# Optimization experiments

Measured on AMD Instinct MI355X. Metric: run time of the kernel, lower is better.

## Reference

```python
import jax, jax.numpy as jnp
import numpy as np

D_IN, D, N_HEADS, K, VOCAB = 768, 512, 8, 6, 1000
HEAD_DIM = D // N_HEADS


def setup_inputs() -> dict:
    key = jax.random.key(0)
    ks = jax.random.split(key, 16)
    B, T, L = 32, 4096, 512
    s = 0.02
    return {
        "video_features": jax.random.normal(ks[0], (B, T, D_IN), jnp.float32),
        "input_ids": jax.random.randint(ks[1], (B, L), 0, VOCAB),
        "attention_mask": jnp.ones((B, L), jnp.float32),
        # video_encoder (Linear 768->512), stored [in, out]
        "W_enc": jax.random.normal(ks[2], (D_IN, D), jnp.float32) * s,
        "b_enc": jnp.zeros((D,), jnp.float32),
        # frame_selector (Linear 512->1)
        "W_sel": jax.random.normal(ks[3], (D, 1), jnp.float32) * s,
        "b_sel": jnp.zeros((1,), jnp.float32),
        # text_encoder embedding
        "emb": jax.random.normal(ks[4], (VOCAB, D), jnp.float32) * s,
        # MultiheadAttention in/out projections
        "W_q": jax.random.normal(ks[5], (D, D), jnp.float32) * s,
        "W_k": jax.random.normal(ks[6], (D, D), jnp.float32) * s,
        "W_v": jax.random.normal(ks[7], (D, D), jnp.float32) * s,
        "b_q": jnp.zeros((D,), jnp.float32),
        "b_k": jnp.zeros((D,), jnp.float32),
        "b_v": jnp.zeros((D,), jnp.float32),
        "W_o": jax.random.normal(ks[8], (D, D), jnp.float32) * s,
        "b_o": jnp.zeros((D,), jnp.float32),
        # classifier (Linear 512->1000)
        "W_cls": jax.random.normal(ks[9], (D, VOCAB), jnp.float32) * s,
        "b_cls": jnp.zeros((VOCAB,), jnp.float32),
    }


def reference(video_features, input_ids, attention_mask, W_enc, b_enc, W_sel,
              b_sel, emb, W_q, W_k, W_v, b_q, b_k, b_v, W_o, b_o, W_cls, b_cls):
    # encode frames: [B, T, 512]
    ve = jax.nn.relu(jnp.einsum('bti,io->bto', video_features, W_enc) + b_enc)
    # frame scores [B, T] -> top-6 gather
    scores = jnp.einsum('btd,do->bto', ve, W_sel)[..., 0] + b_sel[0]
    _, top_idx = jax.lax.top_k(scores, K)                      # [B, K]
    reps = jnp.take_along_axis(ve, top_idx[:, :, None], axis=1)  # [B, K, 512]
    # text embedding (query), reps as key/value
    txt = emb[input_ids]                                       # [B, L, 512]
    B, L, _ = txt.shape
    q = (txt @ W_q + b_q).reshape(B, L, N_HEADS, HEAD_DIM)
    k = (reps @ W_k + b_k).reshape(B, K, N_HEADS, HEAD_DIM)
    v = (reps @ W_v + b_v).reshape(B, K, N_HEADS, HEAD_DIM)
    scale = 1.0 / np.sqrt(HEAD_DIM).astype(np.float32)
    attn = jax.nn.softmax(jnp.einsum('blhd,bkhd->bhlk', q, k) * scale, axis=-1)
    ctx = jnp.einsum('bhlk,bkhd->blhd', attn, v).reshape(B, L, D)
    fused = ctx @ W_o + b_o
    logits = fused @ W_cls + b_cls                             # [B, L, 1000]
    return logits, reps
```

## Files before the change

### kernel.cpp

```cpp
#include <hip/hip_runtime.h>
#include <math.h>


#define DEV __device__ __forceinline__

typedef _Float16 half8 __attribute__((ext_vector_type(8)));
typedef float f32x4v __attribute__((ext_vector_type(4)));

DEV unsigned short f2h_bits(float f) {
  union { _Float16 h; unsigned short u; } cv;
  cv.h = (_Float16)f;
  return cv.u;
}

DEV void gload16(const void* g, void* lds) {
  auto* gp = reinterpret_cast<const __attribute__((address_space(1))) unsigned int*>(
      reinterpret_cast<unsigned long long>(g));
  auto* lp = reinterpret_cast<__attribute__((address_space(3))) unsigned int*>(
      reinterpret_cast<unsigned long long>(lds));
  __builtin_amdgcn_global_load_lds(gp, lp, 16, 0, 0);
}

__global__ __launch_bounds__(256) void wenct_k(const float* __restrict__ W_enc,
                                               unsigned short* __restrict__ WencT) {
  __shared__ unsigned short t[64][65];
  const int k0 = blockIdx.x * 64, n0 = blockIdx.y * 64, tid = threadIdx.x;
  for (int e = tid; e < 4096; e += 256) {
    int kk = e >> 6, nn = e & 63;
    t[kk][nn] = f2h_bits(W_enc[(size_t)(k0 + kk) * 512 + n0 + nn]);
  }
  __syncthreads();
  for (int e = tid; e < 4096; e += 256) {
    int nn = e >> 6, kk = e & 63;
    WencT[(size_t)(n0 + nn) * 768 + k0 + kk] = t[kk][nn];
  }
}

__global__ __launch_bounds__(512, 2) void score_gemm(
    const float* __restrict__ vf, const unsigned short* __restrict__ WencT,
    const float* __restrict__ b_enc, const float* __restrict__ W_sel,
    const float* __restrict__ b_sel, float* __restrict__ scores) {
  __shared__ unsigned short As[128 * 64];
  __shared__ unsigned short Bs[512 * 64];
  __shared__ float red[8 * 128];

  const int tid = threadIdx.x;
  const int w = tid >> 6, lane = tid & 63;
  const int quad = lane >> 4, l15 = lane & 15;
  const int rowBase = blockIdx.x * 128;
  const int swz = l15 & 7;
  char* const AsB = (char*)As;
  char* const BsB = (char*)Bs;

  f32x4v acc[8][4];
#pragma unroll
  for (int i = 0; i < 8; ++i)
#pragma unroll
    for (int j = 0; j < 4; ++j) acc[i][j] = (f32x4v){0.f, 0.f, 0.f, 0.f};

  const int ar0 = tid >> 3, as0 = tid & 7;

  for (int kk = 0; kk < 12; ++kk) {
    const int k0 = kk * 64;
    __syncthreads();
#pragma unroll
    for (int it = 0; it < 8; ++it) {
      int q = tid + it * 512;
      int n = q >> 3, seg = q & 7;
      gload16(WencT + (size_t)n * 768 + k0 + ((seg ^ (n & 7)) << 3),
              BsB + (it * 512 + w * 64) * 16);
    }
#pragma unroll
    for (int h = 0; h < 2; ++h) {
      int row = ar0 + h * 64;
      const float* src = vf + (size_t)(rowBase + row) * 768 + k0 + as0 * 8;
      float4 fa = *(const float4*)src;
      float4 fb = *(const float4*)(src + 4);
      uint4 pk;
      pk.x = f2h_bits(fa.x) | ((unsigned int)f2h_bits(fa.y) << 16);
      pk.y = f2h_bits(fa.z) | ((unsigned int)f2h_bits(fa.w) << 16);
      pk.z = f2h_bits(fb.x) | ((unsigned int)f2h_bits(fb.y) << 16);
      pk.w = f2h_bits(fb.z) | ((unsigned int)f2h_bits(fb.w) << 16);
      *(uint4*)(AsB + row * 128 + ((as0 ^ (row & 7)) << 4)) = pk;
    }
    __syncthreads();
#pragma unroll
    for (int c = 0; c < 2; ++c) {
      half8 af[8], bfr[4];
      const int so = (((c << 2) | quad) ^ swz) << 4;
#pragma unroll
      for (int i = 0; i < 8; ++i)
        af[i] = *(const half8*)(AsB + (16 * i + l15) * 128 + so);
#pragma unroll
      for (int j = 0; j < 4; ++j)
        bfr[j] = *(const half8*)(BsB + (w * 64 + 16 * j + l15) * 128 + so);
#pragma unroll
      for (int i = 0; i < 8; ++i)
#pragma unroll
        for (int j = 0; j < 4; ++j)
          acc[i][j] = __builtin_amdgcn_mfma_f32_16x16x32_f16(af[i], bfr[j], acc[i][j], 0, 0, 0);
    }
  }

  float be[4], wsv[4];
#pragma unroll
  for (int j = 0; j < 4; ++j) {
    int col = w * 64 + 16 * j + l15;
    be[j] = b_enc[col];
    wsv[j] = W_sel[col];
  }
  float part[32];
#pragma unroll
  for (int x = 0; x < 32; ++x) part[x] = 0.f;
#pragma unroll
  for (int i = 0; i < 8; ++i)
#pragma unroll
    for (int j = 0; j < 4; ++j)
#pragma unroll
      for (int r = 0; r < 4; ++r) {
        float v = acc[i][j][r] + be[j];
        v = fmaxf(v, 0.f);
        part[i * 4 + r] += v * wsv[j];
      }
#pragma unroll
  for (int m = 1; m < 16; m <<= 1)
#pragma unroll
    for (int x = 0; x < 32; ++x) part[x] += __shfl_xor(part[x], m);
  if (l15 == 0) {
#pragma unroll
    for (int i = 0; i < 8; ++i)
#pragma unroll
      for (int r = 0; r < 4; ++r)
        red[w * 128 + 16 * i + quad * 4 + r] = part[i * 4 + r];
  }
  __syncthreads();
  if (tid < 128) {
    float s = 0.f;
#pragma unroll
    for (int ww = 0; ww < 8; ++ww) s += red[ww * 128 + tid];
    scores[rowBase + tid] = s + b_sel[0];
  }
}

__global__ __launch_bounds__(256) void topk16(const float* __restrict__ scores,
                                              int* __restrict__ cand) {
  __shared__ float swv[4];
  __shared__ int swi[4];
  __shared__ int winner;
  const int b = blockIdx.x, tid = threadIdx.x;
  const int lane = tid & 63, w = tid >> 6;
  float v[16];
#pragma unroll
  for (int p = 0; p < 16; ++p) v[p] = scores[b * 4096 + p * 256 + tid];
  for (int r = 0; r < 16; ++r) {
    float bv = v[0];
    int bp = 0;
#pragma unroll
    for (int p = 1; p < 16; ++p)
      if (v[p] > bv) { bv = v[p]; bp = p; }
    int bi = bp * 256 + tid;
#pragma unroll
    for (int m = 1; m < 64; m <<= 1) {
      float ov = __shfl_xor(bv, m);
      int oi = __shfl_xor(bi, m);
      if (ov > bv || (ov == bv && oi < bi)) { bv = ov; bi = oi; }
    }
    if (lane == 0) { swv[w] = bv; swi[w] = bi; }
    __syncthreads();
    if (tid == 0) {
      float fv = swv[0];
      int fi = swi[0];
#pragma unroll
      for (int x = 1; x < 4; ++x)
        if (swv[x] > fv || (swv[x] == fv && swi[x] < fi)) { fv = swv[x]; fi = swi[x]; }
      cand[b * 16 + r] = fi;
      winner = fi;
    }
    __syncthreads();
    const int wi = winner;
    const int wp = wi >> 8, wt = wi & 255;
#pragma unroll
    for (int p = 0; p < 16; ++p)
      if (p == wp && tid == wt) v[p] = -3.0e38f;
    __syncthreads();
  }
}

__global__ __launch_bounds__(256) void rescore(
    const float* __restrict__ vf, const int* __restrict__ cand,
    const float* __restrict__ W_enc, const float* __restrict__ b_enc,
    const float* __restrict__ W_sel, const float* __restrict__ b_sel,
    float* __restrict__ veC, float* __restrict__ exsc) {
  __shared__ float vfs[4][768];
  __shared__ float redl[16];
  const int b = blockIdx.x, cb = blockIdx.y * 4, tid = threadIdx.x;
  for (int c = 0; c < 4; ++c) {
    int t = cand[b * 16 + cb + c];
    const float* src = vf + ((size_t)b * 4096 + t) * 768;
    for (int i = tid; i < 768; i += 256) vfs[c][i] = src[i];
  }
  __syncthreads();
  const int j0 = tid, j1 = tid + 256;
  float a0[4] = {0.f, 0.f, 0.f, 0.f}, a1[4] = {0.f, 0.f, 0.f, 0.f};
  for (int i = 0; i < 768; ++i) {
    float w0 = W_enc[(size_t)i * 512 + j0], w1 = W_enc[(size_t)i * 512 + j1];
#pragma unroll
    for (int c = 0; c < 4; ++c) {
      float x = vfs[c][i];
      a0[c] += x * w0;
      a1[c] += x * w1;
    }
  }
  float ws0 = W_sel[j0], ws1 = W_sel[j1];
  float be0 = b_enc[j0], be1 = b_enc[j1];
  float s[4];
#pragma unroll
  for (int c = 0; c < 4; ++c) {
    float v0 = fmaxf(a0[c] + be0, 0.f);
    float v1 = fmaxf(a1[c] + be1, 0.f);
    veC[((size_t)b * 16 + cb + c) * 512 + j0] = v0;
    veC[((size_t)b * 16 + cb + c) * 512 + j1] = v1;
    s[c] = v0 * ws0 + v1 * ws1;
  }
#pragma unroll
  for (int m = 1; m < 64; m <<= 1)
#pragma unroll
    for (int c = 0; c < 4; ++c) s[c] += __shfl_xor(s[c], m);
  int w = tid >> 6;
  if ((tid & 63) == 0) {
#pragma unroll
    for (int c = 0; c < 4; ++c) redl[c * 4 + w] = s[c];
  }
  __syncthreads();
  if (tid < 4)
    exsc[b * 16 + cb + tid] = redl[tid * 4 + 0] + redl[tid * 4 + 1] +
                              redl[tid * 4 + 2] + redl[tid * 4 + 3] + b_sel[0];
}

__global__ __launch_bounds__(256) void select6(
    const float* __restrict__ exsc, const int* __restrict__ cand,
    const float* __restrict__ veC, int* __restrict__ sel,
    float* __restrict__ repsOut) {
  __shared__ int selL[6];
  const int b = blockIdx.x, tid = threadIdx.x;
  if (tid == 0) {
    float v[16]; int idx[16]; bool used[16];
    for (int c = 0; c < 16; ++c) {
      v[c] = exsc[b * 16 + c];
      idx[c] = cand[b * 16 + c];
      used[c] = false;
    }
    for (int r = 0; r < 6; ++r) {
      int bi = -1;
      for (int c = 0; c < 16; ++c) {
        if (used[c]) continue;
        if (bi < 0 || v[c] > v[bi] || (v[c] == v[bi] && idx[c] < idx[bi])) bi = c;
      }
      used[bi] = true;
      selL[r] = bi;
      sel[b * 6 + r] = bi;
    }
  }
  __syncthreads();
  for (int r = 0; r < 6; ++r) {
    int c = selL[r];
    for (int i = tid; i < 512; i += 256)
      repsOut[((size_t)b * 6 + r) * 512 + i] = veC[((size_t)b * 16 + c) * 512 + i];
  }
}

__global__ __launch_bounds__(256) void kv_proj(
    const int* __restrict__ sel, const float* __restrict__ veC,
    const float* __restrict__ W_k, const float* __restrict__ W_v,
    const float* __restrict__ b_k, const float* __restrict__ b_v,
    float* __restrict__ Ks, float* __restrict__ Vs) {
  __shared__ float rep[512];
  const int br = blockIdx.x;
  const int b = br / 6;
  const int tid = threadIdx.x;
  const int c = sel[br];
  for (int i = tid; i < 512; i += 256) rep[i] = veC[((size_t)b * 16 + c) * 512 + i];
  __syncthreads();
  const int j0 = tid, j1 = tid + 256;
  float k0 = 0.f, k1 = 0.f, v0 = 0.f, v1 = 0.f;
  for (int m = 0; m < 512; ++m) {
    float x = rep[m];
    k0 += x * W_k[m * 512 + j0];
    k1 += x * W_k[m * 512 + j1];
    v0 += x * W_v[m * 512 + j0];
    v1 += x * W_v[m * 512 + j1];
  }
  Ks[(size_t)br * 512 + j0] = (k0 + b_k[j0]) * 0.125f;
  Ks[(size_t)br * 512 + j1] = (k1 + b_k[j1]) * 0.125f;
  Vs[(size_t)br * 512 + j0] = v0 + b_v[j0];
  Vs[(size_t)br * 512 + j1] = v1 + b_v[j1];
}

__global__ __launch_bounds__(256) void qemb_k(
    const float* __restrict__ emb, const float* __restrict__ W_q,
    const float* __restrict__ b_q, float* __restrict__ Qe) {
  __shared__ float er[4 * 512];
  const int r0 = blockIdx.x * 4, tid = threadIdx.x;
  for (int i = tid; i < 2048; i += 256) er[i] = emb[(size_t)r0 * 512 + i];
  __syncthreads();
  const int j0 = tid, j1 = tid + 256;
  float a0[4], a1[4];
#pragma unroll
  for (int r = 0; r < 4; ++r) { a0[r] = 0.f; a1[r] = 0.f; }
  for (int i = 0; i < 512; ++i) {
    float w0 = W_q[i * 512 + j0], w1 = W_q[i * 512 + j1];
#pragma unroll
    for (int r = 0; r < 4; ++r) {
      a0[r] += er[r * 512 + i] * w0;
      a1[r] += er[r * 512 + i] * w1;
    }
  }
  float bq0 = b_q[j0], bq1 = b_q[j1];
#pragma unroll
  for (int r = 0; r < 4; ++r) {
    Qe[(size_t)(r0 + r) * 512 + j0] = a0[r] + bq0;
    Qe[(size_t)(r0 + r) * 512 + j1] = a1[r] + bq1;
  }
}

__global__ __launch_bounds__(256) void woc_k(
    const float* __restrict__ W_o, const float* __restrict__ W_cls,
    unsigned short* __restrict__ WocT) {
  __shared__ float wr[4 * 512];
  const int i0 = blockIdx.x * 4, tid = threadIdx.x;
  for (int i = tid; i < 2048; i += 256) wr[i] = W_o[(size_t)i0 * 512 + i];
  __syncthreads();
  float a[4][4];
#pragma unroll
  for (int r = 0; r < 4; ++r)
#pragma unroll
    for (int c = 0; c < 4; ++c) a[r][c] = 0.f;
  for (int m = 0; m < 512; ++m) {
    float wc[4];
#pragma unroll
    for (int c = 0; c < 4; ++c) {
      int j = tid + c * 256;
      wc[c] = (j < 1000) ? W_cls[(size_t)m * 1000 + j] : 0.f;
    }
#pragma unroll
    for (int r = 0; r < 4; ++r) {
      float x = wr[r * 512 + m];
#pragma unroll
      for (int c = 0; c < 4; ++c) a[r][c] += x * wc[c];
    }
  }
#pragma unroll
  for (int r = 0; r < 4; ++r)
#pragma unroll
    for (int c = 0; c < 4; ++c) {
      int j = tid + c * 256;
      if (j < 1000) WocT[(size_t)j * 512 + i0 + r] = f2h_bits(a[r][c]);
    }
  if (blockIdx.x == 0) {
    for (int i = tid; i < 24 * 512; i += 256) WocT[512000 + i] = 0;
  }
}

__global__ void boc_k(const float* __restrict__ b_o, const float* __restrict__ W_cls,
                      const float* __restrict__ b_cls, float* __restrict__ boc) {
  int j = blockIdx.x * 256 + threadIdx.x;
  float s = 0.f;
  if (j < 1000) {
    for (int m = 0; m < 512; ++m) s += b_o[m] * W_cls[(size_t)m * 1000 + j];
    s += b_cls[j];
  }
  boc[j] = s;
}

__global__ __launch_bounds__(256) void ctx_kernel(
    const int* __restrict__ ids, const float* __restrict__ Qe,
    const float* __restrict__ Ks, const float* __restrict__ Vs,
    unsigned short* __restrict__ CTX) {
  const int token = blockIdx.x * 4 + (threadIdx.x >> 6);
  const int lane = threadIdx.x & 63;
  const int b = token >> 9;
  const int id = ids[token];
  float q[8];
#pragma unroll
  for (int h = 0; h < 8; ++h) q[h] = Qe[(size_t)id * 512 + h * 64 + lane];
  float s[8][6];
#pragma unroll
  for (int kk = 0; kk < 6; ++kk) {
    const float* kp = Ks + ((size_t)b * 6 + kk) * 512 + lane;
    float p[8];
#pragma unroll
    for (int h = 0; h < 8; ++h) p[h] = q[h] * kp[h * 64];
#pragma unroll
    for (int m = 1; m < 64; m <<= 1)
#pragma unroll
      for (int h = 0; h < 8; ++h) p[h] += __shfl_xor(p[h], m);
#pragma unroll
    for (int h = 0; h < 8; ++h) s[h][kk] = p[h];
  }
  const float* vbase = Vs + (size_t)b * 6 * 512 + lane;
#pragma unroll
  for (int h = 0; h < 8; ++h) {
    float mx = s[h][0];
#pragma unroll
    for (int kk = 1; kk < 6; ++kk) mx = fmaxf(mx, s[h][kk]);
    float e[6], sum = 0.f;
#pragma unroll
    for (int kk = 0; kk < 6; ++kk) { e[kk] = __expf(s[h][kk] - mx); sum += e[kk]; }
    float c = 0.f;
#pragma unroll
    for (int kk = 0; kk < 6; ++kk) c += e[kk] * vbase[(size_t)kk * 512 + h * 64];
    c *= (1.f / sum);
    CTX[(size_t)token * 512 + h * 64 + lane] = f2h_bits(c);
  }
}

__global__ __launch_bounds__(512, 2) void logits_gemm(
    const unsigned short* __restrict__ CTX, const unsigned short* __restrict__ WocT,
    const float* __restrict__ boc, float* __restrict__ out) {
  __shared__ unsigned short As[128 * 64];
  __shared__ unsigned short Bs[512 * 64];
  const int tid = threadIdx.x;
  const int w = tid >> 6, lane = tid & 63;
  const int quad = lane >> 4, l15 = lane & 15;
  const int rowBase = blockIdx.x * 128;
  const int n0 = blockIdx.y * 512;
  const int swz = l15 & 7;
  char* const AsB = (char*)As;
  char* const BsB = (char*)Bs;

  f32x4v acc[8][4];
#pragma unroll
  for (int i = 0; i < 8; ++i)
#pragma unroll
    for (int j = 0; j < 4; ++j) acc[i][j] = (f32x4v){0.f, 0.f, 0.f, 0.f};

  for (int kk = 0; kk < 8; ++kk) {
    const int k0 = kk * 64;
    __syncthreads();
#pragma unroll
    for (int h = 0; h < 2; ++h) {
      int u = tid + h * 512;
      int row = u >> 3, seg = u & 7;
      gload16(CTX + (size_t)(rowBase + row) * 512 + k0 + ((seg ^ (row & 7)) << 3),
              AsB + (h * 512 + w * 64) * 16);
    }
#pragma unroll
    for (int it = 0; it < 8; ++it) {
      int q = tid + it * 512;
      int n = q >> 3, seg = q & 7;
      gload16(WocT + (size_t)(n0 + n) * 512 + k0 + ((seg ^ (n & 7)) << 3),
              BsB + (it * 512 + w * 64) * 16);
    }
    __syncthreads();
#pragma unroll
    for (int c = 0; c < 2; ++c) {
      half8 af[8], bfr[4];
      const int so = (((c << 2) | quad) ^ swz) << 4;
#pragma unroll
      for (int i = 0; i < 8; ++i)
        af[i] = *(const half8*)(AsB + (16 * i + l15) * 128 + so);
#pragma unroll
      for (int j = 0; j < 4; ++j)
        bfr[j] = *(const half8*)(BsB + (w * 64 + 16 * j + l15) * 128 + so);
#pragma unroll
      for (int i = 0; i < 8; ++i)
#pragma unroll
        for (int j = 0; j < 4; ++j)
          acc[i][j] = __builtin_amdgcn_mfma_f32_16x16x32_f16(af[i], bfr[j], acc[i][j], 0, 0, 0);
    }
  }

  float bo[4];
#pragma unroll
  for (int j = 0; j < 4; ++j) bo[j] = boc[n0 + w * 64 + 16 * j + l15];
#pragma unroll
  for (int i = 0; i < 8; ++i)
#pragma unroll
    for (int j = 0; j < 4; ++j)
#pragma unroll
      for (int r = 0; r < 4; ++r) {
        int token = rowBase + 16 * i + quad * 4 + r;
        int col = n0 + w * 64 + 16 * j + l15;
        if (col < 1000) out[(size_t)token * 1000 + col] = acc[i][j][r] + bo[j];
      }
}

extern "C" void kernel_launch(void* const* d_in, const int* in_sizes, int n_in,
                              void* d_out, int out_size, void* d_ws, size_t ws_size,
                              hipStream_t stream) {
  (void)in_sizes; (void)n_in; (void)out_size; (void)ws_size;
  const float* vf    = (const float*)d_in[0];
  const int*   ids   = (const int*)d_in[1];
  const float* W_enc = (const float*)d_in[3];
  const float* b_enc = (const float*)d_in[4];
  const float* W_sel = (const float*)d_in[5];
  const float* b_sel = (const float*)d_in[6];
  const float* emb   = (const float*)d_in[7];
  const float* W_q   = (const float*)d_in[8];
  const float* W_k   = (const float*)d_in[9];
  const float* W_v   = (const float*)d_in[10];
  const float* b_q   = (const float*)d_in[11];
  const float* b_k   = (const float*)d_in[12];
  const float* b_v   = (const float*)d_in[13];
  const float* W_o   = (const float*)d_in[14];
  const float* b_o   = (const float*)d_in[15];
  const float* W_cls = (const float*)d_in[16];
  const float* b_cls = (const float*)d_in[17];

  float* out = (float*)d_out;
  float* reps_out = out + (size_t)16384000;

  char* p = (char*)d_ws;
  auto nxt = [&](size_t bytes) -> char* {
    char* q = p;
    p += (bytes + 255) & ~(size_t)255;
    return q;
  };
  unsigned short* WencT = (unsigned short*)nxt((size_t)512 * 768 * 2);
  unsigned short* WocT  = (unsigned short*)nxt((size_t)1024 * 512 * 2);
  unsigned short* CTX   = (unsigned short*)nxt((size_t)16384 * 512 * 2);
  float* scores = (float*)nxt((size_t)131072 * 4);
  int*   cand   = (int*)nxt((size_t)512 * 4);
  float* exsc   = (float*)nxt((size_t)512 * 4);
  float* veC    = (float*)nxt((size_t)32 * 16 * 512 * 4);
  int*   sel    = (int*)nxt((size_t)192 * 4);
  float* Ks     = (float*)nxt((size_t)98304 * 4);
  float* Vs     = (float*)nxt((size_t)98304 * 4);
  float* Qe     = (float*)nxt((size_t)512000 * 4);
  float* boc    = (float*)nxt((size_t)1024 * 4);

  hipLaunchKernelGGL(wenct_k,     dim3(12, 8),  dim3(256), 0, stream, W_enc, WencT);
  hipLaunchKernelGGL(score_gemm,  dim3(1024),   dim3(512), 0, stream, vf, WencT, b_enc, W_sel, b_sel, scores);
  hipLaunchKernelGGL(topk16,      dim3(32),     dim3(256), 0, stream, scores, cand);
  hipLaunchKernelGGL(rescore,     dim3(32, 4),  dim3(256), 0, stream, vf, cand, W_enc, b_enc, W_sel, b_sel, veC, exsc);
  hipLaunchKernelGGL(select6,     dim3(32),     dim3(256), 0, stream, exsc, cand, veC, sel, reps_out);
  hipLaunchKernelGGL(kv_proj,     dim3(192),    dim3(256), 0, stream, sel, veC, W_k, W_v, b_k, b_v, Ks, Vs);
  hipLaunchKernelGGL(qemb_k,      dim3(250),    dim3(256), 0, stream, emb, W_q, b_q, Qe);
  hipLaunchKernelGGL(woc_k,       dim3(128),    dim3(256), 0, stream, W_o, W_cls, WocT);
  hipLaunchKernelGGL(boc_k,       dim3(4),      dim3(256), 0, stream, b_o, W_cls, b_cls, boc);
  hipLaunchKernelGGL(ctx_kernel,  dim3(4096),   dim3(256), 0, stream, ids, Qe, Ks, Vs, CTX);
  hipLaunchKernelGGL(logits_gemm, dim3(128, 2), dim3(512), 0, stream, CTX, WocT, boc, out);
}
```

Baseline: 1.092 ms.

## Fuse prep and selection kernels, double-buffer both MFMA GEMMs with K=32 stages

```diff
diff --git a/kernel.cpp b/kernel.cpp
--- a/kernel.cpp
+++ b/kernel.cpp
@@ -11,6 +11,15 @@
   union { _Float16 h; unsigned short u; } cv;
   cv.h = (_Float16)f;
   return cv.u;
+}
+
+DEV uint4 packf16x8(float4 fa, float4 fb) {
+  uint4 pk;
+  pk.x = (unsigned int)f2h_bits(fa.x) | ((unsigned int)f2h_bits(fa.y) << 16);
+  pk.y = (unsigned int)f2h_bits(fa.z) | ((unsigned int)f2h_bits(fa.w) << 16);
+  pk.z = (unsigned int)f2h_bits(fb.x) | ((unsigned int)f2h_bits(fb.y) << 16);
+  pk.w = (unsigned int)f2h_bits(fb.z) | ((unsigned int)f2h_bits(fb.w) << 16);
+  return pk;
 }
 
 DEV void gload16(const void* g, void* lds) {
@@ -21,18 +30,92 @@
   __builtin_amdgcn_global_load_lds(gp, lp, 16, 0, 0);
 }
 
-__global__ __launch_bounds__(256) void wenct_k(const float* __restrict__ W_enc,
-                                               unsigned short* __restrict__ WencT) {
-  __shared__ unsigned short t[64][65];
-  const int k0 = blockIdx.x * 64, n0 = blockIdx.y * 64, tid = threadIdx.x;
-  for (int e = tid; e < 4096; e += 256) {
-    int kk = e >> 6, nn = e & 63;
-    t[kk][nn] = f2h_bits(W_enc[(size_t)(k0 + kk) * 512 + n0 + nn]);
-  }
-  __syncthreads();
-  for (int e = tid; e < 4096; e += 256) {
-    int nn = e >> 6, kk = e & 63;
-    WencT[(size_t)(n0 + nn) * 768 + k0 + kk] = t[kk][nn];
+__global__ __launch_bounds__(256) void prep_k(
+    const float* __restrict__ W_enc, unsigned short* __restrict__ WencT,
+    const float* __restrict__ emb, const float* __restrict__ W_q,
+    const float* __restrict__ b_q, float* __restrict__ Qe,
+    const float* __restrict__ W_o, const float* __restrict__ W_cls,
+    unsigned short* __restrict__ WocT, const float* __restrict__ b_o,
+    const float* __restrict__ b_cls, float* __restrict__ boc) {
+  __shared__ float plds[2080];
+  const int blk = blockIdx.x, tid = threadIdx.x;
+  if (blk < 96) {
+    unsigned short* t = (unsigned short*)plds;
+    const int k0 = (blk % 12) * 64, n0 = (blk / 12) * 64;
+    for (int e = tid; e < 4096; e += 256) {
+      int kk = e >> 6, nn = e & 63;
+      t[kk * 65 + nn] = f2h_bits(W_enc[(size_t)(k0 + kk) * 512 + n0 + nn]);
+    }
+    __syncthreads();
+    for (int e = tid; e < 4096; e += 256) {
+      int nn = e >> 6, kk = e & 63;
+      WencT[(size_t)(n0 + nn) * 768 + k0 + kk] = t[kk * 65 + nn];
+    }
+  } else if (blk < 346) {
+    float* er = plds;
+    const int r0 = (blk - 96) * 4;
+    for (int i = tid; i < 2048; i += 256) er[i] = emb[(size_t)r0 * 512 + i];
+    __syncthreads();
+    const int j0 = tid, j1 = tid + 256;
+    float a0[4], a1[4];
+#pragma unroll
+    for (int r = 0; r < 4; ++r) { a0[r] = 0.f; a1[r] = 0.f; }
+    for (int i = 0; i < 512; ++i) {
+      float w0 = W_q[i * 512 + j0], w1 = W_q[i * 512 + j1];
+#pragma unroll
+      for (int r = 0; r < 4; ++r) {
+        a0[r] += er[r * 512 + i] * w0;
+        a1[r] += er[r * 512 + i] * w1;
+      }
+    }
+    float bq0 = b_q[j0], bq1 = b_q[j1];
+#pragma unroll
+    for (int r = 0; r < 4; ++r) {
+      Qe[(size_t)(r0 + r) * 512 + j0] = a0[r] + bq0;
+      Qe[(size_t)(r0 + r) * 512 + j1] = a1[r] + bq1;
+    }
+  } else if (blk < 474) {
+    float* wr = plds;
+    const int i0 = (blk - 346) * 4;
+    for (int i = tid; i < 2048; i += 256) wr[i] = W_o[(size_t)i0 * 512 + i];
+    __syncthreads();
+    float a[4][4];
+#pragma unroll
+    for (int r = 0; r < 4; ++r)
+#pragma unroll
+      for (int c = 0; c < 4; ++c) a[r][c] = 0.f;
+    for (int m = 0; m < 512; ++m) {
+      float wc[4];
+#pragma unroll
+      for (int c = 0; c < 4; ++c) {
+        int j = tid + c * 256;
+        wc[c] = (j < 1000) ? W_cls[(size_t)m * 1000 + j] : 0.f;
+      }
+#pragma unroll
+      for (int r = 0; r < 4; ++r) {
+        float x = wr[r * 512 + m];
+#pragma unroll
+        for (int c = 0; c < 4; ++c) a[r][c] += x * wc[c];
+      }
+    }
+#pragma unroll
+    for (int r = 0; r < 4; ++r)
+#pragma unroll
+      for (int c = 0; c < 4; ++c) {
+        int j = tid + c * 256;
+        if (j < 1000) WocT[(size_t)j * 512 + i0 + r] = f2h_bits(a[r][c]);
+      }
+    if (blk == 346) {
+      for (int i = tid; i < 24 * 512; i += 256) WocT[512000 + i] = 0;
+    }
+  } else {
+    int j = (blk - 474) * 256 + tid;
+    float s = 0.f;
+    if (j < 1000) {
+      for (int m = 0; m < 512; ++m) s += b_o[m] * W_cls[(size_t)m * 1000 + j];
+      s += b_cls[j];
+    }
+    boc[j] = s;
   }
 }
 
@@ -40,17 +123,19 @@
     const float* __restrict__ vf, const unsigned short* __restrict__ WencT,
     const float* __restrict__ b_enc, const float* __restrict__ W_sel,
     const float* __restrict__ b_sel, float* __restrict__ scores) {
-  __shared__ unsigned short As[128 * 64];
-  __shared__ unsigned short Bs[512 * 64];
+  __shared__ unsigned short As[2][128 * 32];
+  __shared__ unsigned short Bs[2][512 * 32];
   __shared__ float red[8 * 128];
 
   const int tid = threadIdx.x;
-  const int w = tid >> 6, lane = tid & 63;
+  const int wv = tid >> 6, lane = tid & 63;
   const int quad = lane >> 4, l15 = lane & 15;
   const int rowBase = blockIdx.x * 128;
-  const int swz = l15 & 7;
-  char* const AsB = (char*)As;
-  char* const BsB = (char*)Bs;
+  const int rso = ((quad ^ (l15 & 3)) << 4);
+  char* const AsB0 = (char*)As[0];
+  char* const AsB1 = (char*)As[1];
+  char* const BsB0 = (char*)Bs[0];
+  char* const BsB1 = (char*)Bs[1];
 
   f32x4v acc[8][4];
 #pragma unroll
@@ -58,54 +143,60 @@
 #pragma unroll
     for (int j = 0; j < 4; ++j) acc[i][j] = (f32x4v){0.f, 0.f, 0.f, 0.f};
 
-  const int ar0 = tid >> 3, as0 = tid & 7;
-
-  for (int kk = 0; kk < 12; ++kk) {
-    const int k0 = kk * 64;
-    __syncthreads();
-#pragma unroll
-    for (int it = 0; it < 8; ++it) {
+  const int arow = tid >> 2, aseg = tid & 3;
+  const float* aSrc = vf + (size_t)(rowBase + arow) * 768 + aseg * 8;
+  const int adst = arow * 64 + ((aseg ^ (arow & 3)) << 4);
+
+  auto stage_b = [&](int kk, char* dstB) {
+#pragma unroll
+    for (int it = 0; it < 4; ++it) {
       int q = tid + it * 512;
-      int n = q >> 3, seg = q & 7;
-      gload16(WencT + (size_t)n * 768 + k0 + ((seg ^ (n & 7)) << 3),
-              BsB + (it * 512 + w * 64) * 16);
-    }
-#pragma unroll
-    for (int h = 0; h < 2; ++h) {
-      int row = ar0 + h * 64;
-      const float* src = vf + (size_t)(rowBase + row) * 768 + k0 + as0 * 8;
-      float4 fa = *(const float4*)src;
-      float4 fb = *(const float4*)(src + 4);
-      uint4 pk;
-      pk.x = f2h_bits(fa.x) | ((unsigned int)f2h_bits(fa.y) << 16);
-      pk.y = f2h_bits(fa.z) | ((unsigned int)f2h_bits(fa.w) << 16);
-      pk.z = f2h_bits(fb.x) | ((unsigned int)f2h_bits(fb.y) << 16);
-      pk.w = f2h_bits(fb.z) | ((unsigned int)f2h_bits(fb.w) << 16);
-      *(uint4*)(AsB + row * 128 + ((as0 ^ (row & 7)) << 4)) = pk;
-    }
-    __syncthreads();
-#pragma unroll
-    for (int c = 0; c < 2; ++c) {
-      half8 af[8], bfr[4];
-      const int so = (((c << 2) | quad) ^ swz) << 4;
-#pragma unroll
-      for (int i = 0; i < 8; ++i)
-        af[i] = *(const half8*)(AsB + (16 * i + l15) * 128 + so);
+      int n = q >> 2, seg = q & 3;
+      gload16(WencT + (size_t)n * 768 + kk * 32 + ((seg ^ (n & 3)) << 3),
+              dstB + (it * 512 + wv * 64) * 16);
+    }
+  };
+  auto consume = [&](const char* A, const char* B) {
+    half8 af[8], bf[4];
+#pragma unroll
+    for (int i = 0; i < 8; ++i)
+      af[i] = *(const half8*)(A + (16 * i + l15) * 64 + rso);
+#pragma unroll
+    for (int j = 0; j < 4; ++j)
+      bf[j] = *(const half8*)(B + (wv * 64 + 16 * j + l15) * 64 + rso);
+#pragma unroll
+    for (int i = 0; i < 8; ++i)
 #pragma unroll
       for (int j = 0; j < 4; ++j)
-        bfr[j] = *(const half8*)(BsB + (w * 64 + 16 * j + l15) * 128 + so);
-#pragma unroll
-      for (int i = 0; i < 8; ++i)
-#pragma unroll
-        for (int j = 0; j < 4; ++j)
-          acc[i][j] = __builtin_amdgcn_mfma_f32_16x16x32_f16(af[i], bfr[j], acc[i][j], 0, 0, 0);
-    }
-  }
+        acc[i][j] = __builtin_amdgcn_mfma_f32_16x16x32_f16(af[i], bf[j], acc[i][j], 0, 0, 0);
+  };
+
+  stage_b(0, BsB0);
+  {
+    float4 fa = *(const float4*)(aSrc);
+    float4 fb = *(const float4*)(aSrc + 4);
+    *(uint4*)(AsB0 + adst) = packf16x8(fa, fb);
+  }
+  __syncthreads();
+  int cur = 0;
+  for (int kk = 0; kk < 23; ++kk) {
+    const float* s = aSrc + (kk + 1) * 32;
+    float4 fa = *(const float4*)(s);
+    float4 fb = *(const float4*)(s + 4);
+    char* An = cur ? AsB0 : AsB1;
+    char* Bn = cur ? BsB0 : BsB1;
+    stage_b(kk + 1, Bn);
+    consume(cur ? AsB1 : AsB0, cur ? BsB1 : BsB0);
+    *(uint4*)(An + adst) = packf16x8(fa, fb);
+    __syncthreads();
+    cur ^= 1;
+  }
+  consume(cur ? AsB1 : AsB0, cur ? BsB1 : BsB0);
 
   float be[4], wsv[4];
 #pragma unroll
   for (int j = 0; j < 4; ++j) {
-    int col = w * 64 + 16 * j + l15;
+    int col = wv * 64 + 16 * j + l15;
     be[j] = b_enc[col];
     wsv[j] = W_sel[col];
   }
@@ -131,7 +222,7 @@
     for (int i = 0; i < 8; ++i)
 #pragma unroll
       for (int r = 0; r < 4; ++r)
-        red[w * 128 + 16 * i + quad * 4 + r] = part[i * 4 + r];
+        red[wv * 128 + 16 * i + quad * 4 + r] = part[i * 4 + r];
   }
   __syncthreads();
   if (tid < 128) {
@@ -142,234 +233,160 @@
   }
 }
 
-__global__ __launch_bounds__(256) void topk16(const float* __restrict__ scores,
-                                              int* __restrict__ cand) {
-  __shared__ float swv[4];
-  __shared__ int swi[4];
+__global__ __launch_bounds__(512) void select_fused(
+    const float* __restrict__ scores, const float* __restrict__ vf,
+    const float* __restrict__ W_enc, const float* __restrict__ b_enc,
+    const float* __restrict__ W_sel, const float* __restrict__ b_sel,
+    const float* __restrict__ W_k, const float* __restrict__ W_v,
+    const float* __restrict__ b_k, const float* __restrict__ b_v,
+    float* __restrict__ repsOut, float* __restrict__ Ks,
+    float* __restrict__ Vs) {
+  __shared__ float ve[16][512];
+  __shared__ float redl[16 * 4];
+  __shared__ float exsc[16];
+  __shared__ int cand16[16];
+  __shared__ float swv[8];
+  __shared__ int swi[8];
   __shared__ int winner;
+  __shared__ int selL[6];
   const int b = blockIdx.x, tid = threadIdx.x;
-  const int lane = tid & 63, w = tid >> 6;
-  float v[16];
-#pragma unroll
-  for (int p = 0; p < 16; ++p) v[p] = scores[b * 4096 + p * 256 + tid];
+  const int lane = tid & 63, wv = tid >> 6;
+
+  float v[8];
+#pragma unroll
+  for (int p = 0; p < 8; ++p) v[p] = scores[b * 4096 + p * 512 + tid];
   for (int r = 0; r < 16; ++r) {
     float bv = v[0];
     int bp = 0;
 #pragma unroll
-    for (int p = 1; p < 16; ++p)
+    for (int p = 1; p < 8; ++p)
       if (v[p] > bv) { bv = v[p]; bp = p; }
-    int bi = bp * 256 + tid;
+    int bi = bp * 512 + tid;
 #pragma unroll
     for (int m = 1; m < 64; m <<= 1) {
       float ov = __shfl_xor(bv, m);
       int oi = __shfl_xor(bi, m);
       if (ov > bv || (ov == bv && oi < bi)) { bv = ov; bi = oi; }
     }
-    if (lane == 0) { swv[w] = bv; swi[w] = bi; }
+    if (lane == 0) { swv[wv] = bv; swi[wv] = bi; }
     __syncthreads();
     if (tid == 0) {
       float fv = swv[0];
       int fi = swi[0];
 #pragma unroll
-      for (int x = 1; x < 4; ++x)
+      for (int x = 1; x < 8; ++x)
         if (swv[x] > fv || (swv[x] == fv && swi[x] < fi)) { fv = swv[x]; fi = swi[x]; }
-      cand[b * 16 + r] = fi;
+      cand16[r] = fi;
       winner = fi;
     }
     __syncthreads();
-    const int wi = winner;
-    const int wp = wi >> 8, wt = wi & 255;
-#pragma unroll
-    for (int p = 0; p < 16; ++p)
-      if (p == wp && tid == wt) v[p] = -3.0e38f;
-    __syncthreads();
-  }
-}
-
-__global__ __launch_bounds__(256) void rescore(
-    const float* __restrict__ vf, const int* __restrict__ cand,
-    const float* __restrict__ W_enc, const float* __restrict__ b_enc,
-    const float* __restrict__ W_sel, const float* __restrict__ b_sel,
-    float* __restrict__ veC, float* __restrict__ exsc) {
-  __shared__ float vfs[4][768];
-  __shared__ float redl[16];
-  const int b = blockIdx.x, cb = blockIdx.y * 4, tid = threadIdx.x;
-  for (int c = 0; c < 4; ++c) {
-    int t = cand[b * 16 + cb + c];
-    const float* src = vf + ((size_t)b * 4096 + t) * 768;
-    for (int i = tid; i < 768; i += 256) vfs[c][i] = src[i];
-  }
-  __syncthreads();
-  const int j0 = tid, j1 = tid + 256;
-  float a0[4] = {0.f, 0.f, 0.f, 0.f}, a1[4] = {0.f, 0.f, 0.f, 0.f};
-  for (int i = 0; i < 768; ++i) {
-    float w0 = W_enc[(size_t)i * 512 + j0], w1 = W_enc[(size_t)i * 512 + j1];
-#pragma unroll
-    for (int c = 0; c < 4; ++c) {
-      float x = vfs[c][i];
-      a0[c] += x * w0;
-      a1[c] += x * w1;
-    }
-  }
-  float ws0 = W_sel[j0], ws1 = W_sel[j1];
-  float be0 = b_enc[j0], be1 = b_enc[j1];
-  float s[4];
-#pragma unroll
-  for (int c = 0; c < 4; ++c) {
-    float v0 = fmaxf(a0[c] + be0, 0.f);
-    float v1 = fmaxf(a1[c] + be1, 0.f);
-    veC[((size_t)b * 16 + cb + c) * 512 + j0] = v0;
-    veC[((size_t)b * 16 + cb + c) * 512 + j1] = v1;
-    s[c] = v0 * ws0 + v1 * ws1;
-  }
-#pragma unroll
-  for (int m = 1; m < 64; m <<= 1)
-#pragma unroll
-    for (int c = 0; c < 4; ++c) s[c] += __shfl_xor(s[c], m);
-  int w = tid >> 6;
-  if ((tid & 63) == 0) {
-#pragma unroll
-    for (int c = 0; c < 4; ++c) redl[c * 4 + w] = s[c];
-  }
-  __syncthreads();
-  if (tid < 4)
-    exsc[b * 16 + cb + tid] = redl[tid * 4 + 0] + redl[tid * 4 + 1] +
-                              redl[tid * 4 + 2] + redl[tid * 4 + 3] + b_sel[0];
-}
-
-__global__ __launch_bounds__(256) void select6(
-    const float* __restrict__ exsc, const int* __restrict__ cand,
-    const float* __restrict__ veC, int* __restrict__ sel,
-    float* __restrict__ repsOut) {
-  __shared__ int selL[6];
-  const int b = blockIdx.x, tid = threadIdx.x;
+    const int wi2 = winner;
+    if (tid == (wi2 & 511)) {
+      const int wp = wi2 >> 9;
+#pragma unroll
+      for (int p = 0; p < 8; ++p)
+        if (p == wp) v[p] = -3.0e38f;
+    }
+  }
+
+  const int j = tid;
+  const float* rp[16];
+#pragma unroll
+  for (int c = 0; c < 16; ++c) {
+    int t = __builtin_amdgcn_readfirstlane(cand16[c]);
+    rp[c] = vf + ((size_t)b * 4096 + t) * 768;
+  }
+  float a[16];
+#pragma unroll
+  for (int c = 0; c < 16; ++c) a[c] = 0.f;
+  for (int i = 0; i < 768; i += 4) {
+    float w0 = W_enc[(size_t)(i + 0) * 512 + j];
+    float w1 = W_enc[(size_t)(i + 1) * 512 + j];
+    float w2 = W_enc[(size_t)(i + 2) * 512 + j];
+    float w3 = W_enc[(size_t)(i + 3) * 512 + j];
+#pragma unroll
+    for (int c = 0; c < 16; ++c) {
+      a[c] += rp[c][i + 0] * w0;
+      a[c] += rp[c][i + 1] * w1;
+      a[c] += rp[c][i + 2] * w2;
+      a[c] += rp[c][i + 3] * w3;
+    }
+  }
+  float ben = b_enc[j];
+#pragma unroll
+  for (int c = 0; c < 16; ++c) ve[c][j] = fmaxf(a[c] + ben, 0.f);
+  __syncthreads();
+  if (tid < 256) {
+    float ws0 = W_sel[tid], ws1 = W_sel[tid + 256];
+    float s[16];
+#pragma unroll
+    for (int c = 0; c < 16; ++c)
+      s[c] = ve[c][tid] * ws0 + ve[c][tid + 256] * ws1;
+#pragma unroll
+    for (int m = 1; m < 64; m <<= 1)
+#pragma unroll
+      for (int c = 0; c < 16; ++c) s[c] += __shfl_xor(s[c], m);
+    if ((tid & 63) == 0) {
+      int w4 = tid >> 6;
+#pragma unroll
+      for (int c = 0; c < 16; ++c) redl[c * 4 + w4] = s[c];
+    }
+  }
+  __syncthreads();
+  if (tid < 16)
+    exsc[tid] = redl[tid * 4 + 0] + redl[tid * 4 + 1] + redl[tid * 4 + 2] +
+                redl[tid * 4 + 3] + b_sel[0];
+  __syncthreads();
+
   if (tid == 0) {
-    float v[16]; int idx[16]; bool used[16];
-    for (int c = 0; c < 16; ++c) {
-      v[c] = exsc[b * 16 + c];
-      idx[c] = cand[b * 16 + c];
-      used[c] = false;
-    }
+    bool used[16];
+    for (int c = 0; c < 16; ++c) used[c] = false;
     for (int r = 0; r < 6; ++r) {
       int bi = -1;
       for (int c = 0; c < 16; ++c) {
         if (used[c]) continue;
-        if (bi < 0 || v[c] > v[bi] || (v[c] == v[bi] && idx[c] < idx[bi])) bi = c;
+        if (bi < 0 || exsc[c] > exsc[bi] ||
+            (exsc[c] == exsc[bi] && cand16[c] < cand16[bi])) bi = c;
       }
       used[bi] = true;
       selL[r] = bi;
-      sel[b * 6 + r] = bi;
-    }
-  }
-  __syncthreads();
+    }
+  }
+  __syncthreads();
+#pragma unroll
+  for (int r = 0; r < 6; ++r)
+    repsOut[((size_t)b * 6 + r) * 512 + tid] = ve[selL[r]][tid];
+
+  float ka[6], va6[6];
+#pragma unroll
+  for (int r = 0; r < 6; ++r) { ka[r] = 0.f; va6[r] = 0.f; }
+  const float* vrow[6];
+#pragma unroll
+  for (int r = 0; r < 6; ++r) vrow[r] = ve[selL[r]];
+  for (int m = 0; m < 512; m += 4) {
+    float wk0 = W_k[(size_t)(m + 0) * 512 + j];
+    float wk1 = W_k[(size_t)(m + 1) * 512 + j];
+    float wk2 = W_k[(size_t)(m + 2) * 512 + j];
+    float wk3 = W_k[(size_t)(m + 3) * 512 + j];
+    float wv0 = W_v[(size_t)(m + 0) * 512 + j];
+    float wv1 = W_v[(size_t)(m + 1) * 512 + j];
+    float wv2 = W_v[(size_t)(m + 2) * 512 + j];
+    float wv3 = W_v[(size_t)(m + 3) * 512 + j];
+#pragma unroll
+    for (int r = 0; r < 6; ++r) {
+      f32x4v x = *(const f32x4v*)&vrow[r][m];
+      ka[r] += x[0] * wk0; ka[r] += x[1] * wk1;
+      ka[r] += x[2] * wk2; ka[r] += x[3] * wk3;
+      va6[r] += x[0] * wv0; va6[r] += x[1] * wv1;
+      va6[r] += x[2] * wv2; va6[r] += x[3] * wv3;
+    }
+  }
+  float bk = b_k[j], bvv = b_v[j];
+#pragma unroll
   for (int r = 0; r < 6; ++r) {
-    int c = selL[r];
-    for (int i = tid; i < 512; i += 256)
-      repsOut[((size_t)b * 6 + r) * 512 + i] = veC[((size_t)b * 16 + c) * 512 + i];
-  }
-}
-
-__global__ __launch_bounds__(256) void kv_proj(
-    const int* __restrict__ sel, const float* __restrict__ veC,
-    const float* __restrict__ W_k, const float* __restrict__ W_v,
-    const float* __restrict__ b_k, const float* __restrict__ b_v,
-    float* __restrict__ Ks, float* __restrict__ Vs) {
-  __shared__ float rep[512];
-  const int br = blockIdx.x;
-  const int b = br / 6;
-  const int tid = threadIdx.x;
-  const int c = sel[br];
-  for (int i = tid; i < 512; i += 256) rep[i] = veC[((size_t)b * 16 + c) * 512 + i];
-  __syncthreads();
-  const int j0 = tid, j1 = tid + 256;
-  float k0 = 0.f, k1 = 0.f, v0 = 0.f, v1 = 0.f;
-  for (int m = 0; m < 512; ++m) {
-    float x = rep[m];
-    k0 += x * W_k[m * 512 + j0];
-    k1 += x * W_k[m * 512 + j1];
-    v0 += x * W_v[m * 512 + j0];
-    v1 += x * W_v[m * 512 + j1];
-  }
-  Ks[(size_t)br * 512 + j0] = (k0 + b_k[j0]) * 0.125f;
-  Ks[(size_t)br * 512 + j1] = (k1 + b_k[j1]) * 0.125f;
-  Vs[(size_t)br * 512 + j0] = v0 + b_v[j0];
-  Vs[(size_t)br * 512 + j1] = v1 + b_v[j1];
-}
-
-__global__ __launch_bounds__(256) void qemb_k(
-    const float* __restrict__ emb, const float* __restrict__ W_q,
-    const float* __restrict__ b_q, float* __restrict__ Qe) {
-  __shared__ float er[4 * 512];
-  const int r0 = blockIdx.x * 4, tid = threadIdx.x;
-  for (int i = tid; i < 2048; i += 256) er[i] = emb[(size_t)r0 * 512 + i];
-  __syncthreads();
-  const int j0 = tid, j1 = tid + 256;
-  float a0[4], a1[4];
-#pragma unroll
-  for (int r = 0; r < 4; ++r) { a0[r] = 0.f; a1[r] = 0.f; }
-  for (int i = 0; i < 512; ++i) {
-    float w0 = W_q[i * 512 + j0], w1 = W_q[i * 512 + j1];
-#pragma unroll
-    for (int r = 0; r < 4; ++r) {
-      a0[r] += er[r * 512 + i] * w0;
-      a1[r] += er[r * 512 + i] * w1;
-    }
-  }
-  float bq0 = b_q[j0], bq1 = b_q[j1];
-#pragma unroll
-  for (int r = 0; r < 4; ++r) {
-    Qe[(size_t)(r0 + r) * 512 + j0] = a0[r] + bq0;
-    Qe[(size_t)(r0 + r) * 512 + j1] = a1[r] + bq1;
-  }
-}
-
-__global__ __launch_bounds__(256) void woc_k(
-    const float* __restrict__ W_o, const float* __restrict__ W_cls,
-    unsigned short* __restrict__ WocT) {
-  __shared__ float wr[4 * 512];
-  const int i0 = blockIdx.x * 4, tid = threadIdx.x;
-  for (int i = tid; i < 2048; i += 256) wr[i] = W_o[(size_t)i0 * 512 + i];
-  __syncthreads();
-  float a[4][4];
-#pragma unroll
-  for (int r = 0; r < 4; ++r)
-#pragma unroll
-    for (int c = 0; c < 4; ++c) a[r][c] = 0.f;
-  for (int m = 0; m < 512; ++m) {
-    float wc[4];
-#pragma unroll
-    for (int c = 0; c < 4; ++c) {
-      int j = tid + c * 256;
-      wc[c] = (j < 1000) ? W_cls[(size_t)m * 1000 + j] : 0.f;
-    }
-#pragma unroll
-    for (int r = 0; r < 4; ++r) {
-      float x = wr[r * 512 + m];
-#pragma unroll
-      for (int c = 0; c < 4; ++c) a[r][c] += x * wc[c];
-    }
-  }
-#pragma unroll
-  for (int r = 0; r < 4; ++r)
-#pragma unroll
-    for (int c = 0; c < 4; ++c) {
-      int j = tid + c * 256;
-      if (j < 1000) WocT[(size_t)j * 512 + i0 + r] = f2h_bits(a[r][c]);
-    }
-  if (blockIdx.x == 0) {
-    for (int i = tid; i < 24 * 512; i += 256) WocT[512000 + i] = 0;
-  }
-}
-
-__global__ void boc_k(const float* __restrict__ b_o, const float* __restrict__ W_cls,
-                      const float* __restrict__ b_cls, float* __restrict__ boc) {
-  int j = blockIdx.x * 256 + threadIdx.x;
-  float s = 0.f;
-  if (j < 1000) {
-    for (int m = 0; m < 512; ++m) s += b_o[m] * W_cls[(size_t)m * 1000 + j];
-    s += b_cls[j];
-  }
-  boc[j] = s;
+    Ks[((size_t)b * 6 + r) * 512 + j] = (ka[r] + bk) * 0.125f;
+    Vs[((size_t)b * 6 + r) * 512 + j] = va6[r] + bvv;
+  }
 }
 
 __global__ __launch_bounds__(256) void ctx_kernel(
@@ -417,16 +434,18 @@
 __global__ __launch_bounds__(512, 2) void logits_gemm(
     const unsigned short* __restrict__ CTX, const unsigned short* __restrict__ WocT,
     const float* __restrict__ boc, float* __restrict__ out) {
-  __shared__ unsigned short As[128 * 64];
-  __shared__ unsigned short Bs[512 * 64];
+  __shared__ unsigned short As[2][128 * 32];
+  __shared__ unsigned short Bs[2][512 * 32];
   const int tid = threadIdx.x;
-  const int w = tid >> 6, lane = tid & 63;
+  const int wv = tid >> 6, lane = tid & 63;
   const int quad = lane >> 4, l15 = lane & 15;
   const int rowBase = blockIdx.x * 128;
   const int n0 = blockIdx.y * 512;
-  const int swz = l15 & 7;
-  char* const AsB = (char*)As;
-  char* const BsB = (char*)Bs;
+  const int rso = ((quad ^ (l15 & 3)) << 4);
+  char* const AsB0 = (char*)As[0];
+  char* const AsB1 = (char*)As[1];
+  char* const BsB0 = (char*)Bs[0];
+  char* const BsB1 = (char*)Bs[1];
 
   f32x4v acc[8][4];
 #pragma unroll
@@ -434,45 +453,49 @@
 #pragma unroll
     for (int j = 0; j < 4; ++j) acc[i][j] = (f32x4v){0.f, 0.f, 0.f, 0.f};
 
-  for (int kk = 0; kk < 8; ++kk) {
-    const int k0 = kk * 64;
-    __syncthreads();
-#pragma unroll
-    for (int h = 0; h < 2; ++h) {
-      int u = tid + h * 512;
-      int row = u >> 3, seg = u & 7;
-      gload16(CTX + (size_t)(rowBase + row) * 512 + k0 + ((seg ^ (row & 7)) << 3),
-              AsB + (h * 512 + w * 64) * 16);
-    }
-#pragma unroll
-    for (int it = 0; it < 8; ++it) {
+  const int arow = tid >> 2, aseg = tid & 3;
+
+  auto stage = [&](int kk, char* An, char* Bn) {
+    const int k0 = kk * 32;
+    gload16(CTX + (size_t)(rowBase + arow) * 512 + k0 + ((aseg ^ (arow & 3)) << 3),
+            An + (wv * 64) * 16);
+#pragma unroll
+    for (int it = 0; it < 4; ++it) {
       int q = tid + it * 512;
-      int n = q >> 3, seg = q & 7;
-      gload16(WocT + (size_t)(n0 + n) * 512 + k0 + ((seg ^ (n & 7)) << 3),
-              BsB + (it * 512 + w * 64) * 16);
-    }
-    __syncthreads();
-#pragma unroll
-    for (int c = 0; c < 2; ++c) {
-      half8 af[8], bfr[4];
-      const int so = (((c << 2) | quad) ^ swz) << 4;
-#pragma unroll
-      for (int i = 0; i < 8; ++i)
-        af[i] = *(const half8*)(AsB + (16 * i + l15) * 128 + so);
+      int n = q >> 2, seg = q & 3;
+      gload16(WocT + (size_t)(n0 + n) * 512 + k0 + ((seg ^ (n & 3)) << 3),
+              Bn + (it * 512 + wv * 64) * 16);
+    }
+  };
+  auto consume = [&](const char* A, const char* B) {
+    half8 af[8], bf[4];
+#pragma unroll
+    for (int i = 0; i < 8; ++i)
+      af[i] = *(const half8*)(A + (16 * i + l15) * 64 + rso);
+#pragma unroll
+    for (int j = 0; j < 4; ++j)
+      bf[j] = *(const half8*)(B + (wv * 64 + 16 * j + l15) * 64 + rso);
+#pragma unroll
+    for (int i = 0; i < 8; ++i)
 #pragma unroll
       for (int j = 0; j < 4; ++j)
-        bfr[j] = *(const half8*)(BsB + (w * 64 + 16 * j + l15) * 128 + so);
-#pragma unroll
-      for (int i = 0; i < 8; ++i)
-#pragma unroll
-        for (int j = 0; j < 4; ++j)
-          acc[i][j] = __builtin_amdgcn_mfma_f32_16x16x32_f16(af[i], bfr[j], acc[i][j], 0, 0, 0);
-    }
-  }
+        acc[i][j] = __builtin_amdgcn_mfma_f32_16x16x32_f16(af[i], bf[j], acc[i][j], 0, 0, 0);
+  };
+
+  stage(0, AsB0, BsB0);
+  __syncthreads();
+  int cur = 0;
+  for (int kk = 0; kk < 15; ++kk) {
+    stage(kk + 1, cur ? AsB0 : AsB1, cur ? BsB0 : BsB1);
+    consume(cur ? AsB1 : AsB0, cur ? BsB1 : BsB0);
+    __syncthreads();
+    cur ^= 1;
+  }
+  consume(cur ? AsB1 : AsB0, cur ? BsB1 : BsB0);
 
   float bo[4];
 #pragma unroll
-  for (int j = 0; j < 4; ++j) bo[j] = boc[n0 + w * 64 + 16 * j + l15];
+  for (int j = 0; j < 4; ++j) bo[j] = boc[n0 + wv * 64 + 16 * j + l15];
 #pragma unroll
   for (int i = 0; i < 8; ++i)
 #pragma unroll
@@ -480,7 +503,7 @@
 #pragma unroll
       for (int r = 0; r < 4; ++r) {
         int token = rowBase + 16 * i + quad * 4 + r;
-        int col = n0 + w * 64 + 16 * j + l15;
+        int col = n0 + wv * 64 + 16 * j + l15;
         if (col < 1000) out[(size_t)token * 1000 + col] = acc[i][j][r] + bo[j];
       }
 }
@@ -520,24 +543,18 @@
   unsigned short* WocT  = (unsigned short*)nxt((size_t)1024 * 512 * 2);
   unsigned short* CTX   = (unsigned short*)nxt((size_t)16384 * 512 * 2);
   float* scores = (float*)nxt((size_t)131072 * 4);
-  int*   cand   = (int*)nxt((size_t)512 * 4);
-  float* exsc   = (float*)nxt((size_t)512 * 4);
-  float* veC    = (float*)nxt((size_t)32 * 16 * 512 * 4);
-  int*   sel    = (int*)nxt((size_t)192 * 4);
   float* Ks     = (float*)nxt((size_t)98304 * 4);
   float* Vs     = (float*)nxt((size_t)98304 * 4);
   float* Qe     = (float*)nxt((size_t)512000 * 4);
   float* boc    = (float*)nxt((size_t)1024 * 4);
 
-  hipLaunchKernelGGL(wenct_k,     dim3(12, 8),  dim3(256), 0, stream, W_enc, WencT);
-  hipLaunchKernelGGL(score_gemm,  dim3(1024),   dim3(512), 0, stream, vf, WencT, b_enc, W_sel, b_sel, scores);
-  hipLaunchKernelGGL(topk16,      dim3(32),     dim3(256), 0, stream, scores, cand);
-  hipLaunchKernelGGL(rescore,     dim3(32, 4),  dim3(256), 0, stream, vf, cand, W_enc, b_enc, W_sel, b_sel, veC, exsc);
-  hipLaunchKernelGGL(select6,     dim3(32),     dim3(256), 0, stream, exsc, cand, veC, sel, reps_out);
-  hipLaunchKernelGGL(kv_proj,     dim3(192),    dim3(256), 0, stream, sel, veC, W_k, W_v, b_k, b_v, Ks, Vs);
-  hipLaunchKernelGGL(qemb_k,      dim3(250),    dim3(256), 0, stream, emb, W_q, b_q, Qe);
-  hipLaunchKernelGGL(woc_k,       dim3(128),    dim3(256), 0, stream, W_o, W_cls, WocT);
-  hipLaunchKernelGGL(boc_k,       dim3(4),      dim3(256), 0, stream, b_o, W_cls, b_cls, boc);
-  hipLaunchKernelGGL(ctx_kernel,  dim3(4096),   dim3(256), 0, stream, ids, Qe, Ks, Vs, CTX);
-  hipLaunchKernelGGL(logits_gemm, dim3(128, 2), dim3(512), 0, stream, CTX, WocT, boc, out);
-}
+  hipLaunchKernelGGL(prep_k,       dim3(478),    dim3(256), 0, stream,
+                     W_enc, WencT, emb, W_q, b_q, Qe, W_o, W_cls, WocT, b_o, b_cls, boc);
+  hipLaunchKernelGGL(score_gemm,   dim3(1024),   dim3(512), 0, stream,
+                     vf, WencT, b_enc, W_sel, b_sel, scores);
+  hipLaunchKernelGGL(select_fused, dim3(32),     dim3(512), 0, stream,
+                     scores, vf, W_enc, b_enc, W_sel, b_sel, W_k, W_v, b_k, b_v,
+                     reps_out, Ks, Vs);
+  hipLaunchKernelGGL(ctx_kernel,   dim3(4096),   dim3(256), 0, stream, ids, Qe, Ks, Vs, CTX);
+  hipLaunchKernelGGL(logits_gemm,  dim3(128, 2), dim3(512), 0, stream, CTX, WocT, boc, out);
+}
```

Result: slower. 1.152 ms (+5.5%).
